# Kernel optimization log

Hardware: AMD Instinct MI355X
Metric: run time of the kernel (lower is better)

## Reference

```python
import jax, jax.numpy as jnp
import numpy as np

B, N, L, C, K, NL, FF = 8, 2048, 2048, 256, 16, 2, 4
RADIUS = 0.12


def setup_inputs() -> dict:
    key = jax.random.key(0)
    ks = jax.random.split(key, 18)
    s = 0.02
    return {
        "q_xyz": jax.random.uniform(ks[0], (B, N, 3), dtype=jnp.float32),
        "q_feat": jax.random.normal(ks[1], (B, N, C), dtype=jnp.float32),
        "kv_xyz": jax.random.uniform(ks[2], (B, L, 3), dtype=jnp.float32),
        "kv_feat": jax.random.normal(ks[3], (B, L, C), dtype=jnp.float32),
        # PointTransformerConv linears (bias=False in PyG)
        "W_src": jax.random.normal(ks[4], (NL, C, C), dtype=jnp.float32) * s,
        "W_dst": jax.random.normal(ks[5], (NL, C, C), dtype=jnp.float32) * s,
        "W_lin": jax.random.normal(ks[6], (NL, C, C), dtype=jnp.float32) * s,
        # attn_nn = Linear(C,C)+ReLU (MLP plain_last=False)
        "W_attn": jax.random.normal(ks[7], (NL, C, C), dtype=jnp.float32) * s,
        "b_attn": jnp.zeros((NL, C), dtype=jnp.float32),
        # FFN
        "W1": jax.random.normal(ks[8], (NL, C, C * FF), dtype=jnp.float32) * s,
        "b1": jnp.zeros((NL, C * FF), dtype=jnp.float32),
        "W2": jax.random.normal(ks[9], (NL, C * FF, C), dtype=jnp.float32) * s,
        "b2": jnp.zeros((NL, C), dtype=jnp.float32),
        # LayerNorms
        "ln1_g": jnp.ones((NL, C), dtype=jnp.float32),
        "ln1_b": jnp.zeros((NL, C), dtype=jnp.float32),
        "ln2_g": jnp.ones((NL, C), dtype=jnp.float32),
        "ln2_b": jnp.zeros((NL, C), dtype=jnp.float32),
    }


def _ln(x, g, b, eps=1e-5):
    mu = x.mean(-1, keepdims=True)
    var = ((x - mu) ** 2).mean(-1, keepdims=True)
    return (x - mu) * jax.lax.rsqrt(var + eps) * g + b


def reference(q_xyz, q_feat, kv_xyz, kv_feat, W_src, W_dst, W_lin, W_attn,
              b_attn, W1, b1, W2, b2, ln1_g, ln1_b, ln2_g, ln2_b):
    # radius ball query: up to K nearest kv points within RADIUS of each query
    d2 = jnp.sum((q_xyz[:, :, None, :] - kv_xyz[:, None, :, :]) ** 2, axis=-1)  # [B,N,L]
    neg, idx = jax.lax.top_k(-d2, K)            # idx: [B,N,K] into L
    valid = (-neg) <= RADIUS * RADIUS           # [B,N,K] in-ball mask
    vmask = valid[..., None].astype(q_feat.dtype)

    gather = jax.vmap(lambda a, i: a[i])        # [B,L,C],[B,N,K] -> [B,N,K,C]
    out = q_feat
    for i in range(NL):
        a_src = kv_feat @ W_src[i]              # [B,L,C]
        a_dst = out @ W_dst[i]                  # [B,N,C]
        v = kv_feat @ W_lin[i]                  # [B,L,C]
        a_src_g = gather(a_src, idx)            # [B,N,K,C]
        v_g = gather(v, idx)                    # [B,N,K,C]
        # attn_nn(lin_dst(x_i) - lin_src(x_j) + delta), delta=0 (ZeroPos)
        alpha = jax.nn.relu(
            jnp.einsum('bnkc,cd->bnkd', a_dst[:, :, None, :] - a_src_g, W_attn[i]) + b_attn[i])
        logits = jnp.where(valid[..., None], alpha, -1e9)
        attn = jax.nn.softmax(logits, axis=2) * vmask   # per-channel softmax over neighbors
        conv = jnp.sum(attn * v_g, axis=2)              # [B,N,C]
        out = _ln(out + conv, ln1_g[i], ln1_b[i])
        h = jax.nn.gelu(out @ W1[i] + b1[i], approximate=False)
        out = _ln(out + h @ W2[i] + b2[i], ln2_g[i], ln2_b[i])
    return out
```

## Files before the change

### kernel.cpp

```cpp
#include <hip/hip_runtime.h>
#include <math.h>

#define BB 8
#define NN 2048
#define LL 2048
#define CC 256
#define KK 16
#define NL 2
#define FF 4

typedef __attribute__((ext_vector_type(8))) short short8v;
typedef __attribute__((ext_vector_type(4))) float f32x4;

__device__ __forceinline__ short f2b(float f) {
    unsigned u = __float_as_uint(f);
    u += 0x7FFFu + ((u >> 16) & 1u);
    return (short)(u >> 16);
}
__device__ __forceinline__ float b2f(short s) {
    return __uint_as_float(((unsigned)(unsigned short)s) << 16);
}
__device__ __forceinline__ float blo(unsigned u) {
    return __uint_as_float(u << 16);
}
__device__ __forceinline__ float bhi(unsigned u) {
    return __uint_as_float(u & 0xffff0000u);
}

__device__ __forceinline__ void g2l16(const void* g, void* l) {
    __builtin_amdgcn_global_load_lds(
        (const __attribute__((address_space(1))) void*)g,
        (__attribute__((address_space(3))) void*)l, 16, 0, 0);
}

__global__ __launch_bounds__(256) void init_k(const float* __restrict__ src,
                                              float* __restrict__ dst,
                                              short* __restrict__ dstb) {
    size_t i = ((size_t)blockIdx.x * 256 + threadIdx.x) * 4;
    float4 v = *reinterpret_cast<const float4*>(src + i);
    *reinterpret_cast<float4*>(dst + i) = v;
    short o[4] = {f2b(v.x), f2b(v.y), f2b(v.z), f2b(v.w)};
    *reinterpret_cast<int2*>(dstb + i) = *reinterpret_cast<int2*>(o);
}

__global__ __launch_bounds__(256) void f2b_k(const float* __restrict__ in,
                                             short* __restrict__ out) {
    size_t i = ((size_t)blockIdx.x * 256 + threadIdx.x) * 4;
    float4 v = *reinterpret_cast<const float4*>(in + i);
    short o[4] = {f2b(v.x), f2b(v.y), f2b(v.z), f2b(v.w)};
    *reinterpret_cast<int2*>(out + i) = *reinterpret_cast<int2*>(o);
}

__global__ __launch_bounds__(256) void tconvB_k(const float* __restrict__ W0,
                                                short* __restrict__ Wt0,
                                                int K, int N,
                                                size_t sin, size_t sout) {
    const float* W = W0 + (size_t)blockIdx.z * sin;
    short* Wt = Wt0 + (size_t)blockIdx.z * sout;
    __shared__ float tile[32][33];
    const int n0 = blockIdx.x * 32, k0 = blockIdx.y * 32;
    const int tx = threadIdx.x & 31, ty = threadIdx.x >> 5;
#pragma unroll
    for (int r = 0; r < 32; r += 8)
        tile[ty + r][tx] = W[(size_t)(k0 + ty + r) * N + n0 + tx];
    __syncthreads();
#pragma unroll
    for (int r = 0; r < 32; r += 8)
        Wt[(size_t)(n0 + ty + r) * K + k0 + tx] = f2b(tile[tx][ty + r]);
}

#define QPB 32
#define CAP 48
__global__ __launch_bounds__(256) void knn_k(const float* __restrict__ qxyz,
                                             const float* __restrict__ kvxyz,
                                             int* __restrict__ idx,
                                             float* __restrict__ valid) {
    __shared__ float4 sxyz[LL];
    __shared__ unsigned long long cpk[QPB][CAP + 1];
    __shared__ int ccnt[QPB];

    const int t   = threadIdx.x;
    const int q   = t >> 3;
    const int sub = t & 7;
    const int b   = blockIdx.x >> 6;
    const int n   = ((blockIdx.x & 63) << 5) + q;

    const float* kb = kvxyz + (size_t)b * LL * 3;
    for (int p = t; p < LL; p += 256)
        sxyz[p] = make_float4(kb[3 * p], kb[3 * p + 1], kb[3 * p + 2], 0.f);
    if (t < QPB) ccnt[t] = 0;
    __syncthreads();

    const size_t qo = (size_t)(b * NN + n) * 3;
    const float qx = qxyz[qo], qy = qxyz[qo + 1], qz = qxyz[qo + 2];
    const float rad2 = (float)(0.12 * 0.12);

    for (int j = sub; j < LL; j += 32) {
        float4 p0 = sxyz[j];
        float4 p1 = sxyz[j + 8];
        float4 p2 = sxyz[j + 16];
        float4 p3 = sxyz[j + 24];
        float x0 = qx - p0.x, y0 = qy - p0.y, z0 = qz - p0.z;
        float x1 = qx - p1.x, y1 = qy - p1.y, z1 = qz - p1.z;
        float x2 = qx - p2.x, y2 = qy - p2.y, z2 = qz - p2.z;
        float x3 = qx - p3.x, y3 = qy - p3.y, z3 = qz - p3.z;
        float d0 = fmaf(x0, x0, fmaf(y0, y0, z0 * z0));
        float d1 = fmaf(x1, x1, fmaf(y1, y1, z1 * z1));
        float d2 = fmaf(x2, x2, fmaf(y2, y2, z2 * z2));
        float d3 = fmaf(x3, x3, fmaf(y3, y3, z3 * z3));
        if (fminf(fminf(d0, d1), fminf(d2, d3)) <= rad2) {
            if (d0 <= rad2) {
                int s = atomicAdd(&ccnt[q], 1);
                if (s < CAP) cpk[q][s] = ((unsigned long long)__float_as_uint(d0) << 32) | (unsigned)(j);
            }
            if (d1 <= rad2) {
                int s = atomicAdd(&ccnt[q], 1);
                if (s < CAP) cpk[q][s] = ((unsigned long long)__float_as_uint(d1) << 32) | (unsigned)(j + 8);
            }
            if (d2 <= rad2) {
                int s = atomicAdd(&ccnt[q], 1);
                if (s < CAP) cpk[q][s] = ((unsigned long long)__float_as_uint(d2) << 32) | (unsigned)(j + 16);
            }
            if (d3 <= rad2) {
                int s = atomicAdd(&ccnt[q], 1);
                if (s < CAP) cpk[q][s] = ((unsigned long long)__float_as_uint(d3) << 32) | (unsigned)(j + 24);
            }
        }
    }
    __syncthreads();

    int c = ccnt[q]; if (c > CAP) c = CAP;
    const size_t o = (size_t)(b * NN + n) * KK;
#pragma unroll 1
    for (int j = sub; j < c; j += 8) {
        const unsigned long long v = cpk[q][j];
        int rank = 0;
#pragma unroll 1
        for (int i = 0; i < c; ++i) rank += (cpk[q][i] < v) ? 1 : 0;
        if (rank < KK) {
            idx[o + rank]   = (int)(v & 0xffffffffu);
            valid[o + rank] = 1.0f;
        }
    }
#pragma unroll
    for (int k = sub; k < KK; k += 8)
        if (k >= c) { idx[o + k] = 0; valid[o + k] = 0.0f; }
}

template <int ACT, int OBF>
__device__ __forceinline__ void mm_body(short* As, short* Bs,
                                        const short* __restrict__ A,
                                        const short* __restrict__ Bt,
                                        const float* __restrict__ bias,
                                        void* __restrict__ Cout,
                                        int N, int Kd, int bx, int by) {
    const int t = threadIdx.x;
    const int lane = t & 63;
    const int wv = t >> 6;
    const int wr = wv >> 1, wc = wv & 1;
    const int lrow = lane & 15;
    const int kc = lane >> 4;
    const int row0 = by * 128;
    const int col0 = bx * 128;

    f32x4 acc[4][4];
#pragma unroll
    for (int m = 0; m < 4; ++m)
#pragma unroll
        for (int n = 0; n < 4; ++n) acc[m][n] = f32x4{0.f, 0.f, 0.f, 0.f};

    const int r0 = t >> 2, cch = t & 3;
    const int scch = cch ^ ((r0 >> 1) & 3);
    const short* Ap0 = A  + (size_t)(row0 + r0) * Kd + scch * 8;
    const short* Ap1 = A  + (size_t)(row0 + r0 + 64) * Kd + scch * 8;
    const short* Bp0 = Bt + (size_t)(col0 + r0) * Kd + scch * 8;
    const short* Bp1 = Bt + (size_t)(col0 + r0 + 64) * Kd + scch * 8;

    auto STAGE = [&](int buf, int k0) {
        g2l16(Ap0 + k0, As + buf * 4096 + t * 8);
        g2l16(Ap1 + k0, As + buf * 4096 + 2048 + t * 8);
        g2l16(Bp0 + k0, Bs + buf * 4096 + t * 8);
        g2l16(Bp1 + k0, Bs + buf * 4096 + 2048 + t * 8);
    };

    STAGE(0, 0);
    __syncthreads();

    const int nt = Kd >> 5;
    int cur = 0;
    for (int tt = 0; tt < nt; ++tt) {
        if (tt + 1 < nt) STAGE(cur ^ 1, (tt + 1) * 32);
        const short* Ac = As + cur * 4096;
        const short* Bc = Bs + cur * 4096;
        short8v af[4], bf[4];
#pragma unroll
        for (int m = 0; m < 4; ++m) {
            const int ar = wr * 64 + m * 16 + lrow;
            af[m] = *(const short8v*)(Ac + ar * 32 + ((kc ^ ((ar >> 1) & 3)) * 8));
        }
#pragma unroll
        for (int n = 0; n < 4; ++n) {
            const int br = wc * 64 + n * 16 + lrow;
            bf[n] = *(const short8v*)(Bc + br * 32 + ((kc ^ ((br >> 1) & 3)) * 8));
        }
#pragma unroll
        for (int m = 0; m < 4; ++m)
#pragma unroll
            for (int n = 0; n < 4; ++n)
                acc[m][n] = __builtin_amdgcn_mfma_f32_16x16x32_bf16(
                    af[m], bf[n], acc[m][n], 0, 0, 0);
        __syncthreads();
        cur ^= 1;
    }

    float bcol[4];
#pragma unroll
    for (int n = 0; n < 4; ++n)
        bcol[n] = bias ? bias[col0 + wc * 64 + n * 16 + lrow] : 0.f;

#pragma unroll
    for (int m = 0; m < 4; ++m) {
#pragma unroll
        for (int n = 0; n < 4; ++n) {
            const int col = col0 + wc * 64 + n * 16 + lrow;
#pragma unroll
            for (int r = 0; r < 4; ++r) {
                const int row = row0 + wr * 64 + m * 16 + kc * 4 + r;
                float v = acc[m][n][r] + bcol[n];
                if (ACT == 1) v = 0.5f * v * (1.0f + erff(v * 0.70710678118654752f));
                if (OBF) ((short*)Cout)[(size_t)row * N + col] = f2b(v);
                else     ((float*)Cout)[(size_t)row * N + col] = v;
            }
        }
    }
}

template <int ACT, int OBF>
__global__ __launch_bounds__(256) void mm_k(const short* __restrict__ A,
                                            const short* __restrict__ Bt,
                                            const float* __restrict__ bias,
                                            void* __restrict__ Cout,
                                            int M, int N, int Kd) {
    __shared__ __align__(16) short As[2 * 128 * 32];
    __shared__ __align__(16) short Bs[2 * 128 * 32];
    mm_body<ACT, OBF>(As, Bs, A, Bt, bias, Cout, N, Kd, blockIdx.x, blockIdx.y);
    (void)M;
}

__global__ __launch_bounds__(256) void wcomb_k(const short* __restrict__ WatT,
                                               const short* __restrict__ Wdst16,
                                               const short* __restrict__ Wsrc16,
                                               short* __restrict__ WcdT,
                                               short* __restrict__ Wsv) {
    __shared__ __align__(16) short As[2 * 128 * 32];
    __shared__ __align__(16) short Bs[2 * 128 * 32];
    const int z = blockIdx.z, i = z >> 1, sel = z & 1;
    const short* A = WatT + (size_t)i * CC * CC;
    const short* B = (sel ? Wsrc16 : Wdst16) + (size_t)i * CC * CC;
    short* C = sel ? (Wsv + (size_t)i * 2 * CC * CC) : (WcdT + (size_t)i * CC * CC);
    mm_body<0, 1>(As, Bs, A, B, nullptr, C, CC, CC, blockIdx.x, blockIdx.y);
}

#define W2BM 64
__global__ __launch_bounds__(256) void w2ln_k(
    const short* __restrict__ A,
    const short* __restrict__ Bt,
    const float* __restrict__ bias,
    const float* __restrict__ ln_g, const float* __restrict__ ln_b,
    float* __restrict__ out, short* __restrict__ outb) {
    __shared__ __align__(16) short As[2 * W2BM * 32];
    __shared__ __align__(16) short Bs[2 * 256 * 32];
    const int t = threadIdx.x;
    const int lane = t & 63;
    const int wv = t >> 6;
    const int lrow = lane & 15;
    const int kc = lane >> 4;
    const int row0 = blockIdx.x * W2BM;
    const int Kd = CC * FF;

    f32x4 acc[16];
#pragma unroll
    for (int n = 0; n < 16; ++n) acc[n] = f32x4{0.f, 0.f, 0.f, 0.f};

    const int r0 = t >> 2, cch = t & 3;
    const int scch = cch ^ ((r0 >> 1) & 3);
    const short* Ap  = A  + (size_t)(row0 + r0) * Kd + scch * 8;
    const short* Bq0 = Bt + (size_t)(r0      ) * Kd + scch * 8;
    const short* Bq1 = Bt + (size_t)(r0 +  64) * Kd + scch * 8;
    const short* Bq2 = Bt + (size_t)(r0 + 128) * Kd + scch * 8;
    const short* Bq3 = Bt + (size_t)(r0 + 192) * Kd + scch * 8;

    auto STAGE = [&](int buf, int k0) {
        g2l16(Ap  + k0, As + buf * 2048 + t * 8);
        g2l16(Bq0 + k0, Bs + buf * 8192 + t * 8);
        g2l16(Bq1 + k0, Bs + buf * 8192 + 2048 + t * 8);
        g2l16(Bq2 + k0, Bs + buf * 8192 + 4096 + t * 8);
        g2l16(Bq3 + k0, Bs + buf * 8192 + 6144 + t * 8);
    };

    STAGE(0, 0);
    __syncthreads();

    const int nt = Kd >> 5;
    int cur = 0;
    for (int tt = 0; tt < nt; ++tt) {
        if (tt + 1 < nt) STAGE(cur ^ 1, (tt + 1) * 32);
        const short* Ac = As + cur * 2048;
        const short* Bc = Bs + cur * 8192;
        const int ar = wv * 16 + lrow;
        short8v af = *(const short8v*)(Ac + ar * 32 + ((kc ^ ((ar >> 1) & 3)) * 8));
#pragma unroll
        for (int n = 0; n < 16; ++n) {
            const int br = n * 16 + lrow;
            short8v bf = *(const short8v*)(Bc + br * 32 + ((kc ^ ((br >> 1) & 3)) * 8));
            acc[n] = __builtin_amdgcn_mfma_f32_16x16x32_bf16(af, bf, acc[n], 0, 0, 0);
        }
        __syncthreads();
        cur ^= 1;
    }

#pragma unroll
    for (int n = 0; n < 16; ++n) {
        const int col = n * 16 + lrow;
        const float bc = bias[col];
#pragma unroll
        for (int r = 0; r < 4; ++r) {
            const int row = row0 + wv * 16 + kc * 4 + r;
            acc[n][r] += bc + out[(size_t)row * CC + col];
        }
    }
#pragma unroll
    for (int r = 0; r < 4; ++r) {
        float s = 0.f;
#pragma unroll
        for (int n = 0; n < 16; ++n) s += acc[n][r];
        s += __shfl_xor(s, 1); s += __shfl_xor(s, 2);
        s += __shfl_xor(s, 4); s += __shfl_xor(s, 8);
        const float mu = s * (1.0f / 256.0f);
        float q = 0.f;
#pragma unroll
        for (int n = 0; n < 16; ++n) {
            const float d = acc[n][r] - mu;
            q = fmaf(d, d, q);
        }
        q += __shfl_xor(q, 1); q += __shfl_xor(q, 2);
        q += __shfl_xor(q, 4); q += __shfl_xor(q, 8);
        const float rstd = rsqrtf(q * (1.0f / 256.0f) + 1e-5f);
        const int row = row0 + wv * 16 + kc * 4 + r;
#pragma unroll
        for (int n = 0; n < 16; ++n) {
            const int col = n * 16 + lrow;
            const float y = (acc[n][r] - mu) * rstd * ln_g[col] + ln_b[col];
            out[(size_t)row * CC + col] = y;
            outb[(size_t)row * CC + col] = f2b(y);
        }
    }
}

#define AQB 4
__global__ __launch_bounds__(256) void attn_ln_k(
    const short* __restrict__ dw, const short* __restrict__ swv,
    const int* __restrict__ idx, const float* __restrict__ valid,
    const float* __restrict__ bat,
    const float* __restrict__ ln_g, const float* __restrict__ ln_b,
    float* __restrict__ out, short* __restrict__ outb) {
    __shared__ int   sidx[AQB * KK];
    __shared__ float sval[AQB * KK];
    __shared__ __align__(16) float sconv[AQB][CC];
    const int t = threadIdx.x;
    const int b   = blockIdx.x & 7;
    const int blk = blockIdx.x >> 3;
    const int bn0 = b * NN + blk * AQB;
    const size_t boff = (size_t)b * LL;

    if (t < AQB * KK) {
        sidx[t] = idx[(size_t)bn0 * KK + t];
        sval[t] = valid[(size_t)bn0 * KK + t];
    }
    __syncthreads();

    const int cp = (t & 127) * 2;
    const int qh = t >> 7;
    const float bias0 = bat[cp], bias1 = bat[cp + 1];
    const unsigned* swvu = (const unsigned*)swv;

#pragma unroll
    for (int qq = 0; qq < 2; ++qq) {
        const int q = qh * 2 + qq;
        const int bn = bn0 + q;
        const unsigned du = *(const unsigned*)(dw + (size_t)bn * CC + cp);
        const float d0 = blo(du) + bias0;
        const float d1 = bhi(du) + bias1;
        float s0 = 0.f, s1 = 0.f, n0 = 0.f, n1 = 0.f;
#pragma unroll
        for (int k = 0; k < KK; ++k) {
            const int j = sidx[q * KK + k];
            const float vv = sval[q * KK + k];
            const unsigned* rp = swvu + (boff + j) * 512;
            const unsigned su = rp[cp >> 1];
            const unsigned vu = rp[128 + (cp >> 1)];
            const float e0 = vv * __expf(fmaxf(d0 - blo(su), 0.f));
            const float e1 = vv * __expf(fmaxf(d1 - bhi(su), 0.f));
            s0 += e0; s1 += e1;
            n0 = fmaf(e0, blo(vu), n0);
            n1 = fmaf(e1, bhi(vu), n1);
        }
        sconv[q][cp]     = (s0 > 0.f) ? n0 / s0 : 0.f;
        sconv[q][cp + 1] = (s1 > 0.f) ? n1 / s1 : 0.f;
    }
    __syncthreads();

    const int lane = t & 63, w = t >> 6;
    float4 gg = *reinterpret_cast<const float4*>(&ln_g[lane * 4]);
    float4 bb = *reinterpret_cast<const float4*>(&ln_b[lane * 4]);
    {
        const int q = w;
        const size_t base = (size_t)(bn0 + q) * CC + lane * 4;
        float4 x = *reinterpret_cast<const float4*>(&out[base]);
        float4 d = *reinterpret_cast<const float4*>(&sconv[q][lane * 4]);
        float v0 = x.x + d.x, v1 = x.y + d.y, v2 = x.z + d.z, v3 = x.w + d.w;
        float s = v0 + v1 + v2 + v3;
#pragma unroll
        for (int o = 32; o > 0; o >>= 1) s += __shfl_xor(s, o);
        const float mu = s * (1.0f / 256.0f);
        const float t0 = v0 - mu, t1 = v1 - mu, t2 = v2 - mu, t3 = v3 - mu;
        float qv = t0 * t0 + t1 * t1 + t2 * t2 + t3 * t3;
#pragma unroll
        for (int o = 32; o > 0; o >>= 1) qv += __shfl_xor(qv, o);
        const float rstd = rsqrtf(qv * (1.0f / 256.0f) + 1e-5f);
        float4 y;
        y.x = t0 * rstd * gg.x + bb.x;
        y.y = t1 * rstd * gg.y + bb.y;
        y.z = t2 * rstd * gg.z + bb.z;
        y.w = t3 * rstd * gg.w + bb.w;
        *reinterpret_cast<float4*>(&out[base]) = y;
        short o4[4] = {f2b(y.x), f2b(y.y), f2b(y.z), f2b(y.w)};
        *reinterpret_cast<int2*>(outb + base) = *reinterpret_cast<int2*>(o4);
    }
}

extern "C" void kernel_launch(void* const* d_in, const int* in_sizes, int n_in,
                              void* d_out, int out_size, void* d_ws, size_t ws_size,
                              hipStream_t stream) {
    const float* q_xyz   = (const float*)d_in[0];
    const float* q_feat  = (const float*)d_in[1];
    const float* kv_xyz  = (const float*)d_in[2];
    const float* kv_feat = (const float*)d_in[3];
    const float* W_src   = (const float*)d_in[4];
    const float* W_dst   = (const float*)d_in[5];
    const float* W_lin   = (const float*)d_in[6];
    const float* W_attn  = (const float*)d_in[7];
    const float* b_attn  = (const float*)d_in[8];
    const float* W1      = (const float*)d_in[9];
    const float* b1      = (const float*)d_in[10];
    const float* W2      = (const float*)d_in[11];
    const float* b2      = (const float*)d_in[12];
    const float* ln1_g   = (const float*)d_in[13];
    const float* ln1_b   = (const float*)d_in[14];
    const float* ln2_g   = (const float*)d_in[15];
    const float* ln2_b   = (const float*)d_in[16];

    float* out = (float*)d_out;
    char* wsb = (char*)d_ws;
    const size_t MB = (size_t)1 << 20;
    int*   idxb   = (int*)(wsb);
    float* validb = (float*)(wsb + 1 * MB);
    short* kvf16  = (short*)(wsb + 2 * MB);
    short* outb16 = (short*)(wsb + 10 * MB);
    short* dw16   = (short*)(wsb + 18 * MB);
    short* swv2   = (short*)(wsb + 26 * MB);
    short* h16    = (short*)(wsb + 58 * MB);
    short* WatT   = (short*)(wsb + 90 * MB);
    short* Wdst16 = (short*)(wsb + 90 * MB + 256 * 1024);
    short* Wsrc16 = (short*)(wsb + 90 * MB + 512 * 1024);
    short* WcdT   = (short*)(wsb + 90 * MB + 768 * 1024);
    short* Wsv    = (short*)(wsb + 91 * MB);
    short* W1T    = (short*)(wsb + 92 * MB);
    short* W2T    = (short*)(wsb + 93 * MB);

    const int M = BB * NN;

    init_k<<<M * CC / (256 * 4), 256, 0, stream>>>(q_feat, out, outb16);
    f2b_k<<<M * CC / (256 * 4), 256, 0, stream>>>(kv_feat, kvf16);
    f2b_k<<<NL * CC * CC / (256 * 4), 256, 0, stream>>>(W_dst, Wdst16);
    f2b_k<<<NL * CC * CC / (256 * 4), 256, 0, stream>>>(W_src, Wsrc16);
    knn_k<<<BB * (NN / QPB), 256, 0, stream>>>(q_xyz, kv_xyz, idxb, validb);

    tconvB_k<<<dim3(8, 8, NL), 256, 0, stream>>>(W_attn, WatT, CC, CC,
                                                 (size_t)CC * CC, (size_t)CC * CC);
    tconvB_k<<<dim3(8, 8, NL), 256, 0, stream>>>(W_lin, Wsv + CC * CC, CC, CC,
                                                 (size_t)CC * CC, (size_t)2 * CC * CC);
    tconvB_k<<<dim3(32, 8, NL), 256, 0, stream>>>(W1, W1T, CC, CC * FF,
                                                  (size_t)CC * CC * FF, (size_t)CC * CC * FF);
    tconvB_k<<<dim3(8, 32, NL), 256, 0, stream>>>(W2, W2T, CC * FF, CC,
                                                  (size_t)CC * CC * FF, (size_t)CC * CC * FF);
    wcomb_k<<<dim3(2, 2, 2 * NL), 256, 0, stream>>>(WatT, Wdst16, Wsrc16, WcdT, Wsv);

    mm_k<0, 1><<<dim3(8, 128), 256, 0, stream>>>(kvf16, Wsv, nullptr, swv2,
                                                 M, 4 * CC, CC);

    for (int i = 0; i < NL; ++i) {
        const size_t oF = (size_t)i * CC * CC * FF;
        const size_t oC = (size_t)i * CC * CC;
        const float* bat = b_attn + (size_t)i * CC;
        const float* b1p = b1 + (size_t)i * CC * FF;
        const float* b2p = b2 + (size_t)i * CC;

        mm_k<0, 1><<<dim3(2, 128), 256, 0, stream>>>(outb16, WcdT + oC, nullptr, dw16, M, CC, CC);

        attn_ln_k<<<M / AQB, 256, 0, stream>>>(dw16, swv2 + (size_t)i * 512,
                                               idxb, validb, bat,
                                               ln1_g + (size_t)i * CC, ln1_b + (size_t)i * CC,
                                               out, outb16);

        mm_k<1, 1><<<dim3(8, 128), 256, 0, stream>>>(outb16, W1T + oF, b1p, h16, M, CC * FF, CC);
        w2ln_k<<<M / W2BM, 256, 0, stream>>>(h16, W2T + oF, b2p,
                                             ln2_g + (size_t)i * CC, ln2_b + (size_t)i * CC,
                                             out, outb16);
    }
    (void)in_sizes; (void)n_in; (void)out_size; (void)ws_size;
}
```

Before: 289.9 us.

## Use triple-buffered LDS pipeline with partial vmcnt waits in GEMM kernels

Moves the bf16 MFMA GEMM kernels (mm_k, wcomb_k, w2ln_k) from double to triple-buffered LDS staging. Loads now run two k-tiles ahead, and each iteration waits only on the oldest tile's global-to-LDS loads through a partial s_waitcnt vmcnt plus a raw s_barrier, replacing the full __syncthreads drain. The goal is to hide more global load latency behind MFMA work. The cost is 50% more LDS, which may reduce occupancy, and correctness now depends on exact vmcnt counts and LDS visibility without a full barrier fence.

After: 298.7 us. 3.0% more time.

```diff
diff --git a/kernel.cpp b/kernel.cpp
--- a/kernel.cpp
+++ b/kernel.cpp
@@ -183,13 +183,19 @@
         g2l16(Bp1 + k0, Bs + buf * 4096 + 2048 + t * 8);
     };
 
+    const int nt = Kd >> 5;
     STAGE(0, 0);
-    __syncthreads();
-
-    const int nt = Kd >> 5;
+    STAGE(1, 32);
+    asm volatile("s_waitcnt vmcnt(4)" ::: "memory");
+    __builtin_amdgcn_s_barrier();
+
     int cur = 0;
     for (int tt = 0; tt < nt; ++tt) {
-        if (tt + 1 < nt) STAGE(cur ^ 1, (tt + 1) * 32);
+        const int nx = tt + 2;
+        if (nx < nt) {
+            int nb = cur + 2; if (nb >= 3) nb -= 3;
+            STAGE(nb, nx * 32);
+        }
         const short* Ac = As + cur * 4096;
         const short* Bc = Bs + cur * 4096;
         short8v af[4], bf[4];
@@ -209,8 +215,12 @@
             for (int n = 0; n < 4; ++n)
                 acc[m][n] = __builtin_amdgcn_mfma_f32_16x16x32_bf16(
                     af[m], bf[n], acc[m][n], 0, 0, 0);
-        __syncthreads();
-        cur ^= 1;
+        if (tt + 1 < nt) {
+            if (nx < nt) asm volatile("s_waitcnt vmcnt(4)" ::: "memory");
+            else         asm volatile("s_waitcnt vmcnt(0)" ::: "memory");
+            __builtin_amdgcn_s_barrier();
+        }
+        cur = (cur + 1 == 3) ? 0 : cur + 1;
     }
 
     float bcol[4];
@@ -241,8 +251,8 @@
                                             const float* __restrict__ bias,
                                             void* __restrict__ Cout,
                                             int M, int N, int Kd) {
-    __shared__ __align__(16) short As[2 * 128 * 32];
-    __shared__ __align__(16) short Bs[2 * 128 * 32];
+    __shared__ __align__(16) short As[3 * 128 * 32];
+    __shared__ __align__(16) short Bs[3 * 128 * 32];
     mm_body<ACT, OBF>(As, Bs, A, Bt, bias, Cout, N, Kd, blockIdx.x, blockIdx.y);
     (void)M;
 }
@@ -252,8 +262,8 @@
                                                const short* __restrict__ Wsrc16,
                                                short* __restrict__ WcdT,
                                                short* __restrict__ Wsv) {
-    __shared__ __align__(16) short As[2 * 128 * 32];
-    __shared__ __align__(16) short Bs[2 * 128 * 32];
+    __shared__ __align__(16) short As[3 * 128 * 32];
+    __shared__ __align__(16) short Bs[3 * 128 * 32];
     const int z = blockIdx.z, i = z >> 1, sel = z & 1;
     const short* A = WatT + (size_t)i * CC * CC;
     const short* B = (sel ? Wsrc16 : Wdst16) + (size_t)i * CC * CC;
@@ -268,8 +278,8 @@
     const float* __restrict__ bias,
     const float* __restrict__ ln_g, const float* __restrict__ ln_b,
     float* __restrict__ out, short* __restrict__ outb) {
-    __shared__ __align__(16) short As[2 * W2BM * 32];
-    __shared__ __align__(16) short Bs[2 * 256 * 32];
+    __shared__ __align__(16) short As[3 * W2BM * 32];
+    __shared__ __align__(16) short Bs[3 * 256 * 32];
     const int t = threadIdx.x;
     const int lane = t & 63;
     const int wv = t >> 6;
@@ -298,13 +308,19 @@
         g2l16(Bq3 + k0, Bs + buf * 8192 + 6144 + t * 8);
     };
 
+    const int nt = Kd >> 5;
     STAGE(0, 0);
-    __syncthreads();
-
-    const int nt = Kd >> 5;
+    STAGE(1, 32);
+    asm volatile("s_waitcnt vmcnt(5)" ::: "memory");
+    __builtin_amdgcn_s_barrier();
+
     int cur = 0;
     for (int tt = 0; tt < nt; ++tt) {
-        if (tt + 1 < nt) STAGE(cur ^ 1, (tt + 1) * 32);
+        const int nx = tt + 2;
+        if (nx < nt) {
+            int nb = cur + 2; if (nb >= 3) nb -= 3;
+            STAGE(nb, nx * 32);
+        }
         const short* Ac = As + cur * 2048;
         const short* Bc = Bs + cur * 8192;
         const int ar = wv * 16 + lrow;
@@ -315,8 +331,12 @@
             short8v bf = *(const short8v*)(Bc + br * 32 + ((kc ^ ((br >> 1) & 3)) * 8));
             acc[n] = __builtin_amdgcn_mfma_f32_16x16x32_bf16(af, bf, acc[n], 0, 0, 0);
         }
-        __syncthreads();
-        cur ^= 1;
+        if (tt + 1 < nt) {
+            if (nx < nt) asm volatile("s_waitcnt vmcnt(5)" ::: "memory");
+            else         asm volatile("s_waitcnt vmcnt(0)" ::: "memory");
+            __builtin_amdgcn_s_barrier();
+        }
+        cur = (cur + 1 == 3) ? 0 : cur + 1;
     }
 
 #pragma unroll
```
